# Kernel tuning notes

Hardware: AMD Instinct MI355X
Metric: run time of the kernel (lower is better)

## Reference

```python
import jax, jax.numpy as jnp
from jax import lax
import numpy as np

B, C, T, S = 128, 512, 512, 128
L = 2 * S + 1  # blank-extended label length


def _ext_labels(seq, blank):
    # Channel index for each extended-label position s: blank at even s, seq[(s-1)//2] at odd s.
    s = jnp.arange(L)
    l = jnp.maximum(0, (s - 1) // 2)
    return jnp.where(s % 2 == 0, blank, seq[l])


def _alpha_pass(probs, lab):
    # probs: [C, T] per-frame probabilities; lab: [L] extended label channel ids.
    # Faithful to compute_alpha(): per-frame renormalization (Rabiner scaling) and
    # start-window masking (s >= L - 2*(T - t)); entries beyond end = 2t+2 are
    # structurally exact zeros, so summing the full masked column equals the
    # original's windowed sum.
    s = jnp.arange(L)
    p_ext = probs[lab, :].T  # [T, L]
    lab_m2 = jnp.concatenate([jnp.full((2,), -1, lab.dtype), lab[:-2]])
    # s-2 transition allowed only at odd s with non-repeated label (s==1 handled by zero pad).
    mask2 = (s % 2 == 1) & (lab != lab_m2)

    a0 = jnp.zeros(L, probs.dtype).at[0].set(p_ext[0, 0]).at[1].set(p_ext[0, 1])
    c0 = a0.sum()
    a0 = jnp.where(c0 > 0, a0 / c0, a0)

    def step(a_prev, inp):
        t, p_t = inp
        start = jnp.maximum(0, L - 2 * (T - t))
        a1 = jnp.concatenate([jnp.zeros(1, a_prev.dtype), a_prev[:-1]])
        a2 = jnp.concatenate([jnp.zeros(2, a_prev.dtype), a_prev[:-2]])
        a_new = (a_prev + a1 + jnp.where(mask2, a2, 0.0)) * p_t
        a_new = jnp.where(s >= start, a_new, 0.0)
        c = a_new.sum()
        a_new = jnp.where(c > 0, a_new / c, a_new)
        return a_new, a_new

    _, rest = lax.scan(step, a0, (jnp.arange(1, T), p_ext[1:]))
    return jnp.concatenate([a0[None, :], rest], axis=0).T  # [L, T]


def _ctc_single(probs, seq, blank):
    lab = _ext_labels(seq, blank)
    a = _alpha_pass(probs, lab)  # alphas
    # betas: alpha pass on time-reversed probs and reversed labels, then flip both axes
    lab_r = _ext_labels(jnp.flip(seq), blank)
    b = jnp.flip(_alpha_pass(jnp.flip(probs, axis=1), lab_r), axis=(0, 1))
    ab = a * b  # [L, T]
    p_ext = probs[lab, :]  # [L, T]
    lh = (ab / p_ext).sum(0)  # [T]
    return -jnp.sum(jnp.log(lh))


def setup_inputs() -> dict:
    key = jax.random.key(0)
    k1, k2 = jax.random.split(key)
    logits = jax.random.normal(k1, (B, C, T), dtype=jnp.float32)
    params = jax.nn.softmax(logits, axis=1)  # module consumes probabilities
    seq = jax.random.randint(k2, (B, S), 1, C, dtype=jnp.int32)  # labels never equal blank=0
    lengths = jnp.full((B,), 4 * T, dtype=jnp.int32)  # lengths//4 == T == params time dim
    return {"params": params, "seq": seq, "lengths": lengths, "blank": 0}


def reference(params, seq, lengths, blank):
    # lengths//4 == T (static, equals params.shape[2]) for all samples by construction.
    losses = jax.vmap(lambda p, q: _ctc_single(p, q, blank))(params, seq)
    return jnp.sum(losses)
```

## Files before the change

kernel.cpp:

```cpp
#include <hip/hip_runtime.h>
#include <math.h>


#define BB 128
#define CC 512
#define TT 512
#define SS 128
#define LL 257
#define LPADH 260

typedef unsigned int  uint;
typedef unsigned short ushort;

template<int CTRL>
__device__ __forceinline__ float dpp0_f32(float x){
    int v = __builtin_bit_cast(int, x);
    int r = __builtin_amdgcn_update_dpp(0, v, CTRL, 0xF, 0xF, true);
    return __builtin_bit_cast(float, r);
}
__device__ __forceinline__ float shfl_up1_f32(float x){ return dpp0_f32<0x138>(x); }
__device__ __forceinline__ float red8f(float x){
    x += dpp0_f32<0x111>(x);
    x += dpp0_f32<0x112>(x);
    x += dpp0_f32<0x114>(x);
    return x;
}
__device__ __forceinline__ float tail3f(float x){
    x += dpp0_f32<0x118>(x);
    x += dpp0_f32<0x142>(x);
    x += dpp0_f32<0x143>(x);
    return x;
}
__device__ __forceinline__ float full64f(float x){ return tail3f(red8f(x)); }
__device__ __forceinline__ float readlane63_f32(float x){
    int v = __builtin_bit_cast(int, x);
    return __builtin_bit_cast(float, __builtin_amdgcn_readlane(v, 63));
}
__device__ __forceinline__ float pow2if(int e){
    return __builtin_bit_cast(float, (127 + e) << 23);
}
__device__ __forceinline__ uint pk_bf16(float lo, float hi){
    return (__builtin_bit_cast(uint, hi) & 0xFFFF0000u)
         | (__builtin_bit_cast(uint, lo) >> 16);
}
__device__ __forceinline__ float up_lo(uint u){ return __builtin_bit_cast(float, u << 16); }
__device__ __forceinline__ float up_hi(uint u){ return __builtin_bit_cast(float, u & 0xFFFF0000u); }
__device__ __forceinline__ float up_us(ushort u){ return __builtin_bit_cast(float, ((uint)u) << 16); }
template<int CTRL>
__device__ __forceinline__ double dpp0_f64(double x){
    int2 v = __builtin_bit_cast(int2, x);
    int2 r;
    r.x = __builtin_amdgcn_update_dpp(0, v.x, CTRL, 0xF, 0xF, true);
    r.y = __builtin_amdgcn_update_dpp(0, v.y, CTRL, 0xF, 0xF, true);
    return __builtin_bit_cast(double, r);
}
__device__ __forceinline__ double full64d(double x){
    x += dpp0_f64<0x111>(x); x += dpp0_f64<0x112>(x); x += dpp0_f64<0x114>(x);
    x += dpp0_f64<0x118>(x); x += dpp0_f64<0x142>(x); x += dpp0_f64<0x143>(x);
    return x;
}

template<bool REV>
__device__ __forceinline__ void scan_body(
    int b, int l, const float* __restrict__ P, const int* __restrict__ seqg,
    int blank, ushort* __restrict__ W, ushort* __restrict__ W4,
    int* __restrict__ Eb)
{
    const bool is63 = (l == 63);
    const float* Pb = P + (size_t)b * (CC*TT);
    const int* sq = seqg + b*SS;

    int r1, r3; float m1, m3;
    if (!REV) {
        r1 = sq[2*l]; r3 = sq[2*l+1];
        int ip = (l==0) ? 0 : (2*l-1);
        m1 = (l==0) ? 1.f : ((r1 != sq[ip]) ? 1.f : 0.f);
        m3 = (r3 != r1) ? 1.f : 0.f;
    } else {
        r1 = sq[SS-1-2*l]; r3 = sq[SS-2-2*l];
        int ip = (l==0) ? 0 : (SS-2*l);
        m1 = (l==0) ? 1.f : ((r1 != sq[ip]) ? 1.f : 0.f);
        m3 = (r3 != r1) ? 1.f : 0.f;
    }
    const float* pBp = Pb + (size_t)blank*TT;
    const float* p1p = Pb + (size_t)r1*TT;
    const float* p3p = Pb + (size_t)r3*TT;
    ushort* Ww  = W  + (size_t)b*TT*LPADH;
    ushort* W4b = W4 + (size_t)b*TT;
    int* EbB = Eb + b*64;

    const int tm0=(4*l+769)>>1, tm1=(4*l+770)>>1, tm2=(4*l+771)>>1, tm3=(4*l+772)>>1;

    float pbB[8], pb1[8], pb3[8];
    #pragma unroll
    for (int j=0;j<8;++j){
        int pc = REV ? (TT-1-j) : j;
        pbB[j]=pBp[pc]; pb1[j]=p1p[pc]; pb3[j]=p3p[pc];
    }

    float a0=0.f,a1=0.f,a2=0.f,a3=0.f,a4=0.f;
    float scNext = 1.f, Sfull = 0.f;
    const float u0i = (l==0) ? 1.f : 0.f;
    uint sbLo[8], sbHi[8]; float s4f[8];

#define STEP(i, j, FIRSTF, MASKF)                                           \
  {                                                                         \
    float u0,u1,u2,u3,u4;                                                   \
    if (FIRSTF) { u0=u0i; u1=u0i; u2=0.f; u3=0.f; u4=0.f; }                 \
    else {                                                                  \
      float e3u = shfl_up1_f32(a3);                                         \
      u0 = a0 + e3u; u1 = (a1+a0) + m1*e3u; u2 = a2+a1;                     \
      u3 = (a3+a2) + m3*a1; u4 = a4+a3;                                     \
      if (MASKF) {                                                          \
        if ((i) >= tm0) u0 = 0.f;                                           \
        if ((i) >= tm1) u1 = 0.f;                                           \
        if ((i) >= tm2) u2 = 0.f;                                           \
        if ((i) >= tm3) u3 = 0.f;                                           \
      }                                                                     \
    }                                                                       \
    float pB=pbB[j], pq=pb1[j], pr=pb3[j];                                  \
    if ((j)==0) { pB*=scNext; pq*=scNext; pr*=scNext; }                     \
    float n0=u0*pB, n1=u1*pq, n2=u2*pB, n3=u3*pr, n4=u4*pB;                 \
    sbLo[j]=pk_bf16(n0,n1); sbHi[j]=pk_bf16(n2,n3); s4f[j]=n4;              \
    if ((j)==5) {                                                           \
      float part=(n0+n1)+(n2+n3); if (is63) part+=n4;                       \
      Sfull = full64f(part);                                                \
    }                                                                       \
    if ((j)==7) {                                                           \
      float Su = readlane63_f32(Sfull);                                     \
      int ex = (__builtin_bit_cast(int, Su) >> 23) & 0xFF;                  \
      int e = (ex==0) ? 0 : (ex-127);                                       \
      e = e < -120 ? -120 : (e > 120 ? 120 : e);                            \
      scNext = pow2if(-e);                                                  \
      if (REV && l==0 && (i)+1 < TT) EbB[((i)+1)>>3] = e;                   \
    }                                                                       \
    a0=n0; a1=n1; a2=n2; a3=n3; a4=n4;                                      \
    int inx = ((i)+8 < TT) ? (i)+8 : TT-1;                                  \
    int pcn = REV ? (TT-1-inx) : inx;                                       \
    pbB[j]=pBp[pcn]; pb1[j]=p1p[pcn]; pb3[j]=p3p[pcn];                      \
  }

#define GSTORE(i0)                                                          \
  {                                                                         \
    _Pragma("unroll")                                                       \
    for (int j=0;j<8;++j)                                                   \
      *reinterpret_cast<uint2*>(Ww + (size_t)j*LPADH + 4*l)                 \
          = make_uint2(sbLo[j], sbHi[j]);                                   \
    if (is63) {                                                             \
      uint4 pk;                                                             \
      pk.x = pk_bf16(s4f[0], s4f[1]);                                       \
      pk.y = pk_bf16(s4f[2], s4f[3]);                                       \
      pk.z = pk_bf16(s4f[4], s4f[5]);                                       \
      pk.w = pk_bf16(s4f[6], s4f[7]);                                       \
      *reinterpret_cast<uint4*>(W4b + (i0)) = pk;                           \
    }                                                                       \
    Ww += 8*LPADH;                                                          \
  }

    STEP(0,0,true,false)  STEP(1,1,false,false) STEP(2,2,false,false)
    STEP(3,3,false,false) STEP(4,4,false,false) STEP(5,5,false,false)
    STEP(6,6,false,false) STEP(7,7,false,false)
    GSTORE(0)
    for (int i0=8; i0<TT-SS; i0+=8) {
        #pragma unroll
        for (int j=0;j<8;++j) STEP(i0+j, j, false, false)
        GSTORE(i0)
    }
    for (int i0=TT-SS; i0<TT; i0+=8) {
        #pragma unroll
        for (int j=0;j<8;++j) STEP(i0+j, j, false, true)
        GSTORE(i0)
    }
#undef STEP
#undef GSTORE
}

__global__ __launch_bounds__(64, 1)
void ctc_scan(const float* __restrict__ P, const int* __restrict__ seqg,
              const int* __restrict__ blankp, ushort* __restrict__ Wa,
              ushort* __restrict__ Wb, ushort* __restrict__ W4a,
              ushort* __restrict__ W4b, int* __restrict__ Eb)
{
    const int bx = blockIdx.x, l = threadIdx.x;
    const int blank = blankp[0];
    if (bx < BB) scan_body<false>(bx,      l, P, seqg, blank, Wa, W4a, Eb);
    else         scan_body<true >(bx - BB, l, P, seqg, blank, Wb, W4b, Eb);
}

__global__ __launch_bounds__(64)
void ctc_combine(const ushort* __restrict__ Wa, const ushort* __restrict__ Wb,
                 const ushort* __restrict__ W4a, const ushort* __restrict__ W4b,
                 const int* __restrict__ Eb, const int* __restrict__ seqg,
                 double* __restrict__ Lq)
{
    const int b = blockIdx.x, q = blockIdx.y, l = threadIdx.x;
    const bool is63 = (l == 63);
    const int* sq = seqg + b*SS;
    const int r1 = sq[SS-1-2*l], r3 = sq[SS-2-2*l];
    const int ip = (l==0) ? 0 : (SS-2*l);
    const float m1 = (l==0) ? 1.f : ((r1 != sq[ip]) ? 1.f : 0.f);
    const float m3 = (r3 != r1) ? 1.f : 0.f;
    const int tm0=(4*l+769)>>1, tm1=(4*l+770)>>1, tm2=(4*l+771)>>1, tm3=(4*l+772)>>1;

    const ushort* WaB = Wa + (size_t)b*TT*LPADH;
    const ushort* WbB = Wb + (size_t)b*TT*LPADH;
    const ushort* W4aB = W4a + (size_t)b*TT;
    const ushort* W4bB = W4b + (size_t)b*TT;
    const int t0 = q*8;

    float Rcur;
    {
        const ushort* rw = WbB + (size_t)(TT-1-t0)*LPADH;
        uint2 xu = *reinterpret_cast<const uint2*>(rw + 4*l);
        float rnp = (up_lo(xu.x)+up_hi(xu.x))+(up_lo(xu.y)+up_hi(xu.y));
        if (is63) rnp += up_us(W4bB[TT-1-t0]);
        Rcur = full64f(rnp);
    }

    float PmN = 1.f, PmD = 1.f;
    int   Ei  = 0;

    #pragma unroll
    for (int k=0; k<8; ++k) {
        const int t = t0 + k;
        const int i = TT-1-t;
        const ushort* arow = WaB + (size_t)t*LPADH;
        uint2 au = *reinterpret_cast<const uint2*>(arow + (252 - 4*l));
        float av0 = up_lo(au.x), av1 = up_hi(au.x);
        float av2 = up_lo(au.y), av3 = up_hi(au.y);
        float a256 = up_us(W4aB[t]);
        float ar4 = shfl_up1_f32(av0);
        if (l == 0) ar4 = a256;

        float u0,u1,u2,u3,u4, rnext = 0.f;
        if (i > 0) {
            const ushort* rw = WbB + (size_t)(i-1)*LPADH;
            uint2 bu = *reinterpret_cast<const uint2*>(rw + 4*l);
            float bv0 = up_lo(bu.x), bv1 = up_hi(bu.x);
            float bv2 = up_lo(bu.y), bv3 = up_hi(bu.y);
            float b4 = up_us(W4bB[i-1]);
            float e3u = shfl_up1_f32(bv3);
            u0 = bv0 + e3u;
            u1 = (bv1 + bv0) + m1*e3u;
            u2 = bv2 + bv1;
            u3 = (bv3 + bv2) + m3*bv1;
            u4 = b4 + bv3;
            if (i >= TT - SS) {
                if (i >= tm0) u0 = 0.f;
                if (i >= tm1) u1 = 0.f;
                if (i >= tm2) u2 = 0.f;
                if (i >= tm3) u3 = 0.f;
            }
            rnext = (bv0+bv1)+(bv2+bv3);
            if (is63) rnext += b4;
        } else {
            u0 = (l==0)?1.f:0.f; u1 = u0; u2=0.f; u3=0.f; u4=0.f;
        }
        float trp = ar4*u0 + av3*u1 + av2*u2 + av1*u3;
        if (is63) trp += av0*u4;
        float sap = (av1 + av2) + (av3 + ar4);
        if (is63) sap += av0;

        float D  = full64f(trp);
        float S  = full64f(sap);
        float Rn = full64f(rnext);
        if (is63) {
            float dd = fmaxf(D, 1e-37f);
            uint bn = __builtin_bit_cast(uint, dd);
            Ei += (int)((bn >> 23) & 0xFFu) - 127;
            PmN *= __builtin_bit_cast(float, (bn & 0x807FFFFFu) | (127u<<23));
            float sr = fmaxf(S * Rcur, 1e-37f);
            uint bd = __builtin_bit_cast(uint, sr);
            Ei -= (int)((bd >> 23) & 0xFFu) - 127;
            PmD *= __builtin_bit_cast(float, (bd & 0x807FFFFFu) | (127u<<23));
            if (i > 0 && (i & 7) == 0) Ei -= Eb[b*64 + (i>>3)];
        }
        Rcur = Rn;
    }
    if (is63)
        Lq[b*64 + q] = log((double)PmN / (double)PmD) + (double)Ei * M_LN2;
}

__global__ __launch_bounds__(256)
void ctc_final(const double* __restrict__ Lq, float* __restrict__ out)
{
    const int t = threadIdx.x;
    double v = 0.0;
    #pragma unroll
    for (int k=0;k<32;++k) v += Lq[t + 256*k];
    double s = full64d(v);
    __shared__ double w[4];
    if ((t & 63) == 63) w[t>>6] = s;
    __syncthreads();
    if (t == 0) out[0] = (float)(-(w[0]+w[1]+w[2]+w[3]));
}

extern "C" void kernel_launch(void* const* d_in, const int* in_sizes, int n_in,
                              void* d_out, int out_size, void* d_ws, size_t ws_size,
                              hipStream_t stream)
{
    const float* P     = (const float*)d_in[0];
    const int*   seq   = (const int*)  d_in[1];
    const int*   blank = (const int*)  d_in[3];

    ushort* Wa  = (ushort*)d_ws;
    ushort* Wb  = Wa  + (size_t)BB*TT*LPADH;
    ushort* W4a = Wb  + (size_t)BB*TT*LPADH;
    ushort* W4b = W4a + (size_t)BB*TT;
    double* Lq  = (double*)(W4b + (size_t)BB*TT);
    int*    Eb  = (int*)(Lq + (size_t)BB*64);
    (void)ws_size; (void)in_sizes; (void)n_in; (void)out_size;

    ctc_scan<<<2*BB, 64, 0, stream>>>(P, seq, blank, Wa, Wb, W4a, W4b, Eb);
    ctc_combine<<<dim3(BB, 64), 64, 0, stream>>>(Wa, Wb, W4a, W4b, Eb, seq, Lq);
    ctc_final<<<1, 256, 0, stream>>>(Lq, (float*)d_out);
}
```

Baseline: 64.82 us.

## Ping-pong scan recurrence between two wavefronts to overlap stores and loads

The sequential CTC alpha/beta scan now runs with two wavefronts per block. They alternate 8-step time groups, handing the recurrence state and scale factor off through shared memory. While one wave computes a group, the other writes the previous group's bf16 rows to global memory and prefetches probabilities for the next group. This is meant to hide store and load latency off the serial dependency chain, at the cost of a __syncthreads and an LDS state handoff every 8 steps.

```diff
diff --git a/kernel.cpp b/kernel.cpp
--- a/kernel.cpp
+++ b/kernel.cpp
@@ -62,10 +62,14 @@
 
 template<bool REV>
 __device__ __forceinline__ void scan_body(
-    int b, int l, const float* __restrict__ P, const int* __restrict__ seqg,
-    int blank, ushort* __restrict__ W, ushort* __restrict__ W4,
-    int* __restrict__ Eb)
-{
+    int b, int wv, int l, const float* __restrict__ P,
+    const int* __restrict__ seqg, int blank,
+    ushort* __restrict__ W, ushort* __restrict__ W4, int* __restrict__ Eb)
+{
+    __shared__ float4 st4[64];
+    __shared__ float  st1[64];
+    __shared__ float  scSh[1];
+
     const bool is63 = (l == 63);
     const float* Pb = P + (size_t)b * (CC*TT);
     const int* sq = seqg + b*SS;
@@ -85,26 +89,26 @@
     const float* pBp = Pb + (size_t)blank*TT;
     const float* p1p = Pb + (size_t)r1*TT;
     const float* p3p = Pb + (size_t)r3*TT;
-    ushort* Ww  = W  + (size_t)b*TT*LPADH;
-    ushort* W4b = W4 + (size_t)b*TT;
     int* EbB = Eb + b*64;
 
     const int tm0=(4*l+769)>>1, tm1=(4*l+770)>>1, tm2=(4*l+771)>>1, tm3=(4*l+772)>>1;
-
-    float pbB[8], pb1[8], pb3[8];
-    #pragma unroll
-    for (int j=0;j<8;++j){
-        int pc = REV ? (TT-1-j) : j;
-        pbB[j]=pBp[pc]; pb1[j]=p1p[pc]; pb3[j]=p3p[pc];
-    }
 
     float a0=0.f,a1=0.f,a2=0.f,a3=0.f,a4=0.f;
     float scNext = 1.f, Sfull = 0.f;
     const float u0i = (l==0) ? 1.f : 0.f;
+    float pbB[8], pb1[8], pb3[8];
     uint sbLo[8], sbHi[8]; float s4f[8];
 
-#define STEP(i, j, FIRSTF, MASKF)                                           \
+#define LOADPG(gg)                                                          \
+  { _Pragma("unroll")                                                       \
+    for (int j=0;j<8;++j){                                                  \
+      int pc = REV ? (TT-1-((gg)*8+j)) : ((gg)*8+j);                        \
+      pbB[j]=pBp[pc]; pb1[j]=p1p[pc]; pb3[j]=p3p[pc];                       \
+    } }
+
+#define STEP(g, j, FIRSTF, MASKF)                                           \
   {                                                                         \
+    const int i = (g)*8 + (j);                                              \
     float u0,u1,u2,u3,u4;                                                   \
     if (FIRSTF) { u0=u0i; u1=u0i; u2=0.f; u3=0.f; u4=0.f; }                 \
     else {                                                                  \
@@ -112,10 +116,10 @@
       u0 = a0 + e3u; u1 = (a1+a0) + m1*e3u; u2 = a2+a1;                     \
       u3 = (a3+a2) + m3*a1; u4 = a4+a3;                                     \
       if (MASKF) {                                                          \
-        if ((i) >= tm0) u0 = 0.f;                                           \
-        if ((i) >= tm1) u1 = 0.f;                                           \
-        if ((i) >= tm2) u2 = 0.f;                                           \
-        if ((i) >= tm3) u3 = 0.f;                                           \
+        if (i >= tm0) u0 = 0.f;                                             \
+        if (i >= tm1) u1 = 0.f;                                             \
+        if (i >= tm2) u2 = 0.f;                                             \
+        if (i >= tm3) u3 = 0.f;                                             \
       }                                                                     \
     }                                                                       \
     float pB=pbB[j], pq=pb1[j], pr=pb3[j];                                  \
@@ -132,16 +136,19 @@
       int e = (ex==0) ? 0 : (ex-127);                                       \
       e = e < -120 ? -120 : (e > 120 ? 120 : e);                            \
       scNext = pow2if(-e);                                                  \
-      if (REV && l==0 && (i)+1 < TT) EbB[((i)+1)>>3] = e;                   \
+      if (REV && l==0 && (g)+1 < 64) EbB[(g)+1] = e;                        \
     }                                                                       \
     a0=n0; a1=n1; a2=n2; a3=n3; a4=n4;                                      \
-    int inx = ((i)+8 < TT) ? (i)+8 : TT-1;                                  \
-    int pcn = REV ? (TT-1-inx) : inx;                                       \
-    pbB[j]=pBp[pcn]; pb1[j]=p1p[pcn]; pb3[j]=p3p[pcn];                      \
   }
 
-#define GSTORE(i0)                                                          \
+#define RGROUP(g, FIRSTF, MASKF)                                            \
+    STEP(g,0,FIRSTF,MASKF) STEP(g,1,false,MASKF) STEP(g,2,false,MASKF)      \
+    STEP(g,3,false,MASKF)  STEP(g,4,false,MASKF) STEP(g,5,false,MASKF)      \
+    STEP(g,6,false,MASKF)  STEP(g,7,false,MASKF)
+
+#define STOREROWS(gg)                                                       \
   {                                                                         \
+    ushort* Ww = W + ((size_t)b*TT + (size_t)(gg)*8) * LPADH;               \
     _Pragma("unroll")                                                       \
     for (int j=0;j<8;++j)                                                   \
       *reinterpret_cast<uint2*>(Ww + (size_t)j*LPADH + 4*l)                 \
@@ -152,39 +159,51 @@
       pk.y = pk_bf16(s4f[2], s4f[3]);                                       \
       pk.z = pk_bf16(s4f[4], s4f[5]);                                       \
       pk.w = pk_bf16(s4f[6], s4f[7]);                                       \
-      *reinterpret_cast<uint4*>(W4b + (i0)) = pk;                           \
+      *reinterpret_cast<uint4*>(W4 + (size_t)b*TT + (size_t)(gg)*8) = pk;   \
     }                                                                       \
-    Ww += 8*LPADH;                                                          \
   }
 
-    STEP(0,0,true,false)  STEP(1,1,false,false) STEP(2,2,false,false)
-    STEP(3,3,false,false) STEP(4,4,false,false) STEP(5,5,false,false)
-    STEP(6,6,false,false) STEP(7,7,false,false)
-    GSTORE(0)
-    for (int i0=8; i0<TT-SS; i0+=8) {
-        #pragma unroll
-        for (int j=0;j<8;++j) STEP(i0+j, j, false, false)
-        GSTORE(i0)
+    LOADPG(wv)
+
+    for (int g = 0; g < 64; ++g) {
+        if ((g & 1) == wv) {
+            if (g > 0) {
+                float4 v = st4[l];
+                a0 = v.x; a1 = v.y; a2 = v.z; a3 = v.w;
+                a4 = st1[l];
+                scNext = scSh[0];
+            }
+            if (g == 0)      { RGROUP(0, true,  false) }
+            else if (g < 48) { RGROUP(g, false, false) }
+            else             { RGROUP(g, false, true ) }
+            st4[l] = make_float4(a0, a1, a2, a3);
+            st1[l] = a4;
+            if (l == 0) scSh[0] = scNext;
+        } else {
+            if (g >= 1) STOREROWS(g-1)
+            if (g >= 1 && g < 63) LOADPG(g+1)
+        }
+        __syncthreads();
     }
-    for (int i0=TT-SS; i0<TT; i0+=8) {
-        #pragma unroll
-        for (int j=0;j<8;++j) STEP(i0+j, j, false, true)
-        GSTORE(i0)
-    }
+    if (wv == 1) STOREROWS(63)
+
 #undef STEP
-#undef GSTORE
-}
-
-__global__ __launch_bounds__(64, 1)
+#undef RGROUP
+#undef STOREROWS
+#undef LOADPG
+}
+
+__global__ __launch_bounds__(128, 1)
 void ctc_scan(const float* __restrict__ P, const int* __restrict__ seqg,
               const int* __restrict__ blankp, ushort* __restrict__ Wa,
               ushort* __restrict__ Wb, ushort* __restrict__ W4a,
               ushort* __restrict__ W4b, int* __restrict__ Eb)
 {
-    const int bx = blockIdx.x, l = threadIdx.x;
+    const int bx = blockIdx.x;
+    const int wv = threadIdx.x >> 6, l = threadIdx.x & 63;
     const int blank = blankp[0];
-    if (bx < BB) scan_body<false>(bx,      l, P, seqg, blank, Wa, W4a, Eb);
-    else         scan_body<true >(bx - BB, l, P, seqg, blank, Wb, W4b, Eb);
+    if (bx < BB) scan_body<false>(bx,      wv, l, P, seqg, blank, Wa, W4a, Eb);
+    else         scan_body<true >(bx - BB, wv, l, P, seqg, blank, Wb, W4b, Eb);
 }
 
 __global__ __launch_bounds__(64)
@@ -311,7 +330,7 @@
     int*    Eb  = (int*)(Lq + (size_t)BB*64);
     (void)ws_size; (void)in_sizes; (void)n_in; (void)out_size;
 
-    ctc_scan<<<2*BB, 64, 0, stream>>>(P, seq, blank, Wa, Wb, W4a, W4b, Eb);
+    ctc_scan<<<2*BB, 128, 0, stream>>>(P, seq, blank, Wa, Wb, W4a, W4b, Eb);
     ctc_combine<<<dim3(BB, 64), 64, 0, stream>>>(Wa, Wb, W4a, W4b, Eb, seq, Lq);
     ctc_final<<<1, 256, 0, stream>>>(Lq, (float*)d_out);
 }
```

Result: no change. 65.18 us (+0.6%).
